# Kernel tuning notes

Measured on AMD Instinct MI355X. Metric: run time of the kernel, lower is better.

The kernel has to match this reference:

```python
import jax, jax.numpy as jnp
import numpy as np

B, C = 2048, 512          # batch, channels
CHG = 16                  # coarse grid side (16x16 -> N=256)
FHG = 16                  # fine grid side (16x16 -> F=256)
N = CHG * CHG             # coarse_span.total
F = FHG * FHG             # fine_total
K = 4                     # top4 sample mode
LOG_F = float(np.log(F))


def _ln(x, g, b, eps=1e-5):
    m = jnp.mean(x, axis=-1, keepdims=True)
    v = jnp.var(x, axis=-1, keepdims=True)
    return (x - m) * jax.lax.rsqrt(v + eps) * g + b


def _mlp3(x, w1, b1, w2, b2, w3, b3):
    # linear_stack: Linear+gelu, Linear+gelu, Linear (dropout=0 / eval)
    h = jax.nn.gelu(x @ w1 + b1)
    h = jax.nn.gelu(h @ w2 + b2)
    return h @ w3 + b3


def setup_inputs() -> dict:
    key = jax.random.key(0)
    ks = jax.random.split(key, 10)
    s = 0.02
    return {
        'x': jax.random.normal(ks[0], (B, C), jnp.float32),
        'in_g': jnp.ones((C,), jnp.float32), 'in_b': jnp.zeros((C,), jnp.float32),
        'nop_w': jax.random.normal(ks[1], (C, 1), jnp.float32) * s,
        'nop_b': jnp.zeros((1,), jnp.float32),
        'c_w1': jax.random.normal(ks[2], (C, C), jnp.float32) * s,
        'c_b1': jnp.zeros((C,), jnp.float32),
        'c_w2': jax.random.normal(ks[3], (C, C), jnp.float32) * s,
        'c_b2': jnp.zeros((C,), jnp.float32),
        'c_w3': jax.random.normal(ks[4], (C, N), jnp.float32) * s,
        'c_b3': jnp.zeros((N,), jnp.float32),
        'emb': jax.random.normal(ks[5], (N, C), jnp.float32),
        'emb_g': jnp.ones((C,), jnp.float32), 'emb_b': jnp.zeros((C,), jnp.float32),
        'f_w1': jax.random.normal(ks[6], (2 * C, C), jnp.float32) * s,
        'f_b1': jnp.zeros((C,), jnp.float32),
        'f_w2': jax.random.normal(ks[7], (C, C), jnp.float32) * s,
        'f_b2': jnp.zeros((C,), jnp.float32),
        'f_w3': jax.random.normal(ks[8], (C, F), jnp.float32) * s,
        'f_b3': jnp.zeros((F,), jnp.float32),
    }


def reference(x, in_g, in_b, nop_w, nop_b, c_w1, c_b1, c_w2, c_b2, c_w3, c_b3,
              emb, emb_g, emb_b, f_w1, f_b1, f_w2, f_b2, f_w3, f_b3):
    xn = _ln(x, in_g, in_b)                                  # (B,C)
    no_op = xn @ nop_w + nop_b                               # (B,1)
    coarse = _mlp3(xn, c_w1, c_b1, c_w2, c_b2, c_w3, c_b3)   # (B,N)
    _, idx = jax.lax.top_k(coarse, K)                        # (B,K) int32
    e = _ln(emb[idx], emb_g, emb_b)                          # (B,K,C)
    fin = jnp.concatenate([jnp.broadcast_to(xn[:, None, :], (B, K, C)), e], axis=-1)
    fine = _mlp3(fin, f_w1, f_b1, f_w2, f_b2, f_w3, f_b3)    # (B,K,F)
    # scatter value: coarse[b,i] - log F + fine + log F - lse(fine) = coarse[b,i] + log_softmax(fine)
    vals = jnp.take_along_axis(coarse, idx, axis=1)[:, :, None] + jax.nn.log_softmax(fine, axis=-1)
    dense = jnp.broadcast_to((coarse - LOG_F)[:, :, None], (B, N, F))
    dense = dense.at[jnp.arange(B)[:, None], idx].set(vals)  # top-k indices are distinct
    # view (B, ch0, ch1, fh0, fh1) -> permute (0,1,3,2,4) -> flatten
    xname = dense.reshape(B, CHG, CHG, FHG, FHG).transpose(0, 1, 3, 2, 4).reshape(B, -1)
    return jnp.concatenate([no_op, xname], axis=-1)          # (B, 1 + N*F)
```

## Files before the change

### kernel.cpp

```cpp
#include <hip/hip_runtime.h>
#include <math.h>

#define BATCH 2048
#define CH 512
#define N_COARSE 256
#define F_FINE 256
#define K_TOP 4
#define OUT_STRIDE 65537

typedef unsigned short ushort_t;
typedef __bf16 bf16x8 __attribute__((ext_vector_type(8)));
typedef float f32x4 __attribute__((ext_vector_type(4)));

typedef __attribute__((address_space(3))) unsigned int lds_uint;
typedef __attribute__((address_space(1))) unsigned int gl_uint;

__device__ __forceinline__ void gload_lds16(const ushort_t* g, ushort_t* l) {
    __builtin_amdgcn_global_load_lds((const gl_uint*)g, (lds_uint*)l, 16, 0, 0);
}

__device__ __forceinline__ float gelu_tanh(float x) {
    float x3 = x * x * x;
    float t = tanhf(0.7978845608028654f * (x + 0.044715f * x3));
    return 0.5f * x * (1.0f + t);
}

__device__ __forceinline__ ushort_t f2bf(float f) {
    unsigned u = __float_as_uint(f);
    unsigned r = (u + 0x7FFF + ((u >> 16) & 1)) >> 16;
    return (ushort_t)r;
}
__device__ __forceinline__ float bf2f(ushort_t h) {
    return __uint_as_float(((unsigned)h) << 16);
}

struct Params {
    const float *x, *in_g, *in_b, *nop_w, *nop_b;
    const float *c_w1, *c_b1, *c_w2, *c_b2, *c_w3, *c_b3;
    const float *emb, *emb_g, *emb_b;
    const float *f_w1, *f_b1, *f_w2, *f_b2, *f_w3, *f_b3;
    float *coarse, *out, *cvals;
    ushort_t *xnsp, *h1sp, *h2sp, *e_bf, *fh1_bf, *fh2_bf;
    ushort_t *wt1, *wt2, *wt3, *cwt1, *cwt2, *cwt3;
    int *idxb;
};

__global__ __launch_bounds__(256) void prep_kernel(Params p) {
    __shared__ float s[32][33];
    int u = blockIdx.x, t = threadIdx.x;
    if (u < 1536) {
        const float* W; ushort_t* Wt; int Kd, Nd, gx, gy; bool split;
        if (u < 512)       { W=p.f_w1; Wt=p.wt1; Kd=1024; Nd=512; gx=u&15; gy=u>>4; split=false; }
        else if (u < 768)  { int v=u-512;  W=p.f_w2; Wt=p.wt2; Kd=512; Nd=512; gx=v&15; gy=v>>4; split=false; }
        else if (u < 896)  { int v=u-768;  W=p.f_w3; Wt=p.wt3; Kd=512; Nd=256; gx=v&7;  gy=v>>3; split=false; }
        else if (u < 1152) { int v=u-896;  W=p.c_w1; Wt=p.cwt1; Kd=512; Nd=512; gx=v&15; gy=v>>4; split=true; }
        else if (u < 1408) { int v=u-1152; W=p.c_w2; Wt=p.cwt2; Kd=512; Nd=512; gx=v&15; gy=v>>4; split=true; }
        else               { int v=u-1408; W=p.c_w3; Wt=p.cwt3; Kd=512; Nd=256; gx=v&7;  gy=v>>3; split=true; }
        int tx = t & 31, ty = t >> 5;
        int n0 = gx * 32, k0 = gy * 32;
        #pragma unroll
        for (int i = 0; i < 4; ++i) {
            int r = ty + i * 8;
            s[r][tx] = W[(size_t)(k0 + r) * Nd + n0 + tx];
        }
        __syncthreads();
        if (!split) {
            #pragma unroll
            for (int i = 0; i < 4; ++i) {
                int r = ty + i * 8;
                Wt[(size_t)(n0 + r) * Kd + k0 + tx] = f2bf(s[tx][r]);
            }
        } else {
            #pragma unroll
            for (int i = 0; i < 4; ++i) {
                int r = ty + i * 8;
                float v = s[tx][r];
                ushort_t h = f2bf(v);
                Wt[(size_t)(n0 + r) * 1024 + k0 + tx] = h;
                Wt[(size_t)(n0 + r) * 1024 + 512 + k0 + tx] = f2bf(v - bf2f(h));
            }
        }
    } else {
        float* red = &s[0][0];
        int row = u - 1536;
        int lane = t & 63, wave = t >> 6;
        const float* xr = p.x + (size_t)row * CH;
        float v0 = xr[t], v1 = xr[t + 256];
        float sm = v0 + v1, ss = v0 * v0 + v1 * v1;
        #pragma unroll
        for (int off = 32; off; off >>= 1) { sm += __shfl_xor(sm, off); ss += __shfl_xor(ss, off); }
        if (lane == 0) { red[wave] = sm; red[4 + wave] = ss; }
        __syncthreads();
        sm = red[0] + red[1] + red[2] + red[3];
        ss = red[4] + red[5] + red[6] + red[7];
        float mean = sm * (1.0f / CH);
        float var = ss * (1.0f / CH) - mean * mean;
        float rsq = rsqrtf(var + 1e-5f);
        float xn0 = (v0 - mean) * rsq * p.in_g[t] + p.in_b[t];
        float xn1 = (v1 - mean) * rsq * p.in_g[t + 256] + p.in_b[t + 256];
        ushort_t* xr2 = p.xnsp + (size_t)row * 1024;
        ushort_t h0 = f2bf(xn0), h1v = f2bf(xn1);
        xr2[t] = h0; xr2[t + 256] = h1v;
        xr2[512 + t] = f2bf(xn0 - bf2f(h0));
        xr2[512 + t + 256] = f2bf(xn1 - bf2f(h1v));
        float d = xn0 * p.nop_w[t] + xn1 * p.nop_w[t + 256];
        #pragma unroll
        for (int off = 32; off; off >>= 1) d += __shfl_xor(d, off);
        __syncthreads();
        if (lane == 0) red[wave] = d;
        __syncthreads();
        if (t == 0) p.out[(size_t)row * OUT_STRIDE] = red[0] + red[1] + red[2] + red[3] + p.nop_b[0];
    }
}

template<bool SKIP>
__device__ __forceinline__ void bg_scatter_unit(const float* __restrict__ coarse,
                                                const int* __restrict__ idxb,
                                                float* __restrict__ out, int gu) {
    const float LOG_F = 5.545177444479562f;
    int b = gu >> 4, cx = gu & 15, t = threadIdx.x;
    int4 ii = SKIP ? *(const int4*)&idxb[b * 4] : make_int4(-1, -1, -1, -1);
    size_t rowb = (size_t)b * OUT_STRIDE + 1;
    const float* cr = coarse + (size_t)b * N_COARSE;
    #pragma unroll
    for (int q = 0; q < 4; ++q) {
        int o = cx * 4096 + q * 1024 + t * 4;
        int n = ((o >> 12) << 4) | ((o >> 4) & 15);
        bool skip = SKIP && ((n == ii.x) | (n == ii.y) | (n == ii.z) | (n == ii.w));
        if (!skip) {
            float base = cr[n] - LOG_F;
            float* op = out + rowb + o;
            __builtin_nontemporal_store(base, op + 0);
            __builtin_nontemporal_store(base, op + 1);
            __builtin_nontemporal_store(base, op + 2);
            __builtin_nontemporal_store(base, op + 3);
        }
    }
}

template<int MODE, int MT, int NT, int OUTM>
__global__ __launch_bounds__(256) void mfma_gemm_kernel(
    const ushort_t* __restrict__ A1, const ushort_t* __restrict__ A2,
    const ushort_t* __restrict__ Wt, const float* __restrict__ bias,
    const float* __restrict__ cvals, void* __restrict__ Cout, int Nd, int Ktot,
    const float* __restrict__ coarseB, const int* __restrict__ idxbB,
    float* __restrict__ outB, int gemmY, int suBase)
{
    if ((int)blockIdx.y >= gemmY) {
        int gu = suBase + ((int)blockIdx.y - gemmY) * (int)gridDim.x + (int)blockIdx.x;
        bg_scatter_unit<true>(coarseB, idxbB, outB, gu);
        return;
    }
    constexpr int FI = MT / 32, FJ = NT / 32;
    __shared__ ushort_t As[2][MT * 32];
    __shared__ ushort_t Bs[2][NT * 32];
    __shared__ float mxs[64 * 2];
    __shared__ float ses[64 * 2];
    int t = threadIdx.x;
    int n0 = blockIdx.x * NT, m0 = blockIdx.y * MT;
    int wave = t >> 6, lane = t & 63;
    int wm = (wave & 1) * (MT / 2), wn = (wave >> 1) * (NT / 2);
    int lr = lane & 15, quad = lane >> 4;
    int wbase = wave * 64;

    f32x4 acc[FI][FJ] = {};

    auto stageAB = [&](int k0, int pp) {
        int aoff = (MODE == 2) ? ((k0 >= 1024) ? k0 - 512 : (k0 & 511)) : k0;
        int woff = (MODE == 2) ? ((k0 >= 1024) ? k0 - 1024 : k0) : k0;
        constexpr int AL = MT * 4;
        constexpr int BL = NT * 4;
        if constexpr (AL >= 256) {
            #pragma unroll
            for (int i = 0; i < AL / 256; ++i) {
                int c = i * 256 + t, r = c >> 2, q = (c & 3) * 8;
                int gr = m0 + r;
                const ushort_t* ap;
                if (MODE == 1)      ap = (k0 < 512) ? A1 + (size_t)(gr >> 2) * 1024 + k0 + q
                                                    : A2 + (size_t)gr * 512 + (k0 - 512) + q;
                else if (MODE == 2) ap = A1 + (size_t)gr * 1024 + aoff + q;
                else                ap = A1 + (size_t)gr * Ktot + k0 + q;
                gload_lds16(ap, &As[pp][(i * 256 + wbase) * 8]);
            }
        } else {
            if (t < AL) {
                int c = t, r = c >> 2, q = (c & 3) * 8;
                int gr = m0 + r;
                const ushort_t* ap;
                if (MODE == 1)      ap = (k0 < 512) ? A1 + (size_t)(gr >> 2) * 1024 + k0 + q
                                                    : A2 + (size_t)gr * 512 + (k0 - 512) + q;
                else if (MODE == 2) ap = A1 + (size_t)gr * 1024 + aoff + q;
                else                ap = A1 + (size_t)gr * Ktot + k0 + q;
                gload_lds16(ap, &As[pp][wbase * 8]);
            }
        }
        if constexpr (BL >= 256) {
            #pragma unroll
            for (int i = 0; i < BL / 256; ++i) {
                int c = i * 256 + t, r = c >> 2, q = (c & 3) * 8;
                size_t wstride = (MODE == 2) ? 1024 : (size_t)Ktot;
                const ushort_t* bp = Wt + (size_t)(n0 + r) * wstride + woff + q;
                gload_lds16(bp, &Bs[pp][(i * 256 + wbase) * 8]);
            }
        } else {
            if (t < BL) {
                int c = t, r = c >> 2, q = (c & 3) * 8;
                size_t wstride = (MODE == 2) ? 1024 : (size_t)Ktot;
                const ushort_t* bp = Wt + (size_t)(n0 + r) * wstride + woff + q;
                gload_lds16(bp, &Bs[pp][wbase * 8]);
            }
        }
    };

    stageAB(0, 0);
    int steps = Ktot >> 5;
    int p = 0;
    for (int s = 0; s < steps; ++s) {
        __syncthreads();
        if (s + 1 < steps) stageAB((s + 1) * 32, p ^ 1);
        bf16x8 af[FI], bfr[FJ];
        #pragma unroll
        for (int i = 0; i < FI; ++i)
            af[i] = *(const bf16x8*)&As[p][(wm + i * 16 + lr) * 32 + quad * 8];
        #pragma unroll
        for (int j = 0; j < FJ; ++j)
            bfr[j] = *(const bf16x8*)&Bs[p][(wn + j * 16 + lr) * 32 + quad * 8];
        #pragma unroll
        for (int i = 0; i < FI; ++i)
            #pragma unroll
            for (int j = 0; j < FJ; ++j)
                acc[i][j] = __builtin_amdgcn_mfma_f32_16x16x32_bf16(af[i], bfr[j], acc[i][j], 0, 0, 0);
        p ^= 1;
    }

    if (OUTM == 3) {
        float bv[FJ];
        #pragma unroll
        for (int j = 0; j < FJ; ++j) bv[j] = bias[wn + j * 16 + lr];
        int half = wave >> 1;
        float rmx[FI][4];
        #pragma unroll
        for (int i = 0; i < FI; ++i)
            #pragma unroll
            for (int r = 0; r < 4; ++r) {
                float m = -1e30f;
                #pragma unroll
                for (int j = 0; j < FJ; ++j) m = fmaxf(m, acc[i][j][r] + bv[j]);
                #pragma unroll
                for (int mk = 1; mk < 16; mk <<= 1) m = fmaxf(m, __shfl_xor(m, mk));
                if (lr == 0) mxs[(wm + i * 16 + quad * 4 + r) * 2 + half] = m;
            }
        __syncthreads();
        #pragma unroll
        for (int i = 0; i < FI; ++i)
            #pragma unroll
            for (int r = 0; r < 4; ++r) {
                int rl = wm + i * 16 + quad * 4 + r;
                rmx[i][r] = fmaxf(mxs[rl * 2], mxs[rl * 2 + 1]);
            }
        #pragma unroll
        for (int i = 0; i < FI; ++i)
            #pragma unroll
            for (int r = 0; r < 4; ++r) {
                float sv = 0.f;
                #pragma unroll
                for (int j = 0; j < FJ; ++j) sv += expf(acc[i][j][r] + bv[j] - rmx[i][r]);
                #pragma unroll
                for (int mk = 1; mk < 16; mk <<= 1) sv += __shfl_xor(sv, mk);
                if (lr == 0) ses[(wm + i * 16 + quad * 4 + r) * 2 + half] = sv;
            }
        __syncthreads();
        #pragma unroll
        for (int i = 0; i < FI; ++i)
            #pragma unroll
            for (int r = 0; r < 4; ++r) {
                int rl = wm + i * 16 + quad * 4 + r;
                float se = ses[rl * 2] + ses[rl * 2 + 1];
                float addc = cvals[m0 + rl] - rmx[i][r] - logf(se);
                int m = m0 + rl;
                int n = idxbB[m];
                size_t base = (size_t)(m >> 2) * OUT_STRIDE + 1
                            + (size_t)((n >> 4) * 4096 + (n & 15) * 16);
                #pragma unroll
                for (int j = 0; j < FJ; ++j)
                    __builtin_nontemporal_store(acc[i][j][r] + bv[j] + addc,
                        &outB[base + (size_t)((wn >> 4) + j) * 256 + lr]);
            }
    } else {
        #pragma unroll
        for (int j = 0; j < FJ; ++j) {
            int col = n0 + wn + j * 16 + lr;
            float bvv = bias[col];
            #pragma unroll
            for (int i = 0; i < FI; ++i) {
                #pragma unroll
                for (int r = 0; r < 4; ++r) {
                    int row = m0 + wm + i * 16 + quad * 4 + r;
                    float val = acc[i][j][r] + bvv;
                    if (OUTM == 0) {
                        ((ushort_t*)Cout)[(size_t)row * Nd + col] = f2bf(gelu_tanh(val));
                    } else if (OUTM == 1) {
                        float gv = gelu_tanh(val);
                        ushort_t h = f2bf(gv);
                        ((ushort_t*)Cout)[(size_t)row * 1024 + col] = h;
                        ((ushort_t*)Cout)[(size_t)row * 1024 + 512 + col] = f2bf(gv - bf2f(h));
                    } else {
                        ((float*)Cout)[(size_t)row * Nd + col] = val;
                    }
                }
            }
        }
    }
}

__global__ __launch_bounds__(256) void topk_embln_kernel(Params p, int realX) {
    if ((int)blockIdx.x >= realX) {
        bg_scatter_unit<false>(p.coarse, nullptr, p.out, (int)blockIdx.x - realX);
        return;
    }
    __shared__ int sidx[4];
    int brow = blockIdx.x, t = threadIdx.x;
    int wave = t >> 6, lane = t & 63;
    if (wave == 0) {
        const float* cr = p.coarse + (size_t)brow * N_COARSE;
        float v[4]; int id[4];
        #pragma unroll
        for (int j = 0; j < 4; ++j) { v[j] = cr[lane + 64 * j]; id[j] = lane + 64 * j; }
        #pragma unroll
        for (int r = 0; r < K_TOP; ++r) {
            float bv = v[0]; int bi = id[0];
            #pragma unroll
            for (int j = 1; j < 4; ++j)
                if (v[j] > bv || (v[j] == bv && id[j] < bi)) { bv = v[j]; bi = id[j]; }
            #pragma unroll
            for (int off = 32; off; off >>= 1) {
                float ov = __shfl_xor(bv, off); int oi = __shfl_xor(bi, off);
                if (ov > bv || (ov == bv && oi < bi)) { bv = ov; bi = oi; }
            }
            if ((bi & 63) == lane) v[bi >> 6] = -INFINITY;
            if (lane == 0) {
                sidx[r] = bi;
                p.idxb[brow * K_TOP + r] = bi;
                p.cvals[brow * K_TOP + r] = bv;
            }
        }
    }
    __syncthreads();
    int n = sidx[wave];
    const float* er = p.emb + (size_t)n * CH + lane * 8;
    float4 u0 = *(const float4*)er;
    float4 u1 = *(const float4*)(er + 4);
    float s  = u0.x + u0.y + u0.z + u0.w + u1.x + u1.y + u1.z + u1.w;
    float ss = u0.x * u0.x + u0.y * u0.y + u0.z * u0.z + u0.w * u0.w
             + u1.x * u1.x + u1.y * u1.y + u1.z * u1.z + u1.w * u1.w;
    #pragma unroll
    for (int off = 32; off; off >>= 1) { s += __shfl_xor(s, off); ss += __shfl_xor(ss, off); }
    float mean = s * (1.0f / CH);
    float var = ss * (1.0f / CH) - mean * mean;
    float rsq = rsqrtf(var + 1e-5f);
    float4 g0 = *(const float4*)(p.emb_g + lane * 8), g1 = *(const float4*)(p.emb_g + lane * 8 + 4);
    float4 b0 = *(const float4*)(p.emb_b + lane * 8), b1 = *(const float4*)(p.emb_b + lane * 8 + 4);
    uint4 pk;
    pk.x = (unsigned)f2bf((u0.x - mean) * rsq * g0.x + b0.x) |
           ((unsigned)f2bf((u0.y - mean) * rsq * g0.y + b0.y) << 16);
    pk.y = (unsigned)f2bf((u0.z - mean) * rsq * g0.z + b0.z) |
           ((unsigned)f2bf((u0.w - mean) * rsq * g0.w + b0.w) << 16);
    pk.z = (unsigned)f2bf((u1.x - mean) * rsq * g1.x + b1.x) |
           ((unsigned)f2bf((u1.y - mean) * rsq * g1.y + b1.y) << 16);
    pk.w = (unsigned)f2bf((u1.z - mean) * rsq * g1.z + b1.z) |
           ((unsigned)f2bf((u1.w - mean) * rsq * g1.w + b1.w) << 16);
    *(uint4*)(p.e_bf + (size_t)(brow * K_TOP + wave) * CH + lane * 8) = pk;
}

extern "C" void kernel_launch(void* const* d_in, const int* in_sizes, int n_in,
                              void* d_out, int out_size, void* d_ws, size_t ws_size,
                              hipStream_t stream) {
    Params prm;
    prm.x     = (const float*)d_in[0];
    prm.in_g  = (const float*)d_in[1];
    prm.in_b  = (const float*)d_in[2];
    prm.nop_w = (const float*)d_in[3];
    prm.nop_b = (const float*)d_in[4];
    prm.c_w1  = (const float*)d_in[5];
    prm.c_b1  = (const float*)d_in[6];
    prm.c_w2  = (const float*)d_in[7];
    prm.c_b2  = (const float*)d_in[8];
    prm.c_w3  = (const float*)d_in[9];
    prm.c_b3  = (const float*)d_in[10];
    prm.emb   = (const float*)d_in[11];
    prm.emb_g = (const float*)d_in[12];
    prm.emb_b = (const float*)d_in[13];
    prm.f_w1  = (const float*)d_in[14];
    prm.f_b1  = (const float*)d_in[15];
    prm.f_w2  = (const float*)d_in[16];
    prm.f_b2  = (const float*)d_in[17];
    prm.f_w3  = (const float*)d_in[18];
    prm.f_b3  = (const float*)d_in[19];

    float* ws = (float*)d_ws;
    prm.coarse  = ws;
    prm.xnsp    = (ushort_t*)(prm.coarse + 524288);
    prm.h1sp    = prm.xnsp + 2097152;
    prm.h2sp    = prm.h1sp + 2097152;
    prm.e_bf    = prm.h2sp + 2097152;
    prm.fh1_bf  = prm.e_bf + 4194304;
    prm.fh2_bf  = prm.fh1_bf + 4194304;
    prm.wt1     = prm.fh2_bf + 4194304;
    prm.wt2     = prm.wt1 + 524288;
    prm.wt3     = prm.wt2 + 262144;
    prm.cwt1    = prm.wt3 + 131072;
    prm.cwt2    = prm.cwt1 + 524288;
    prm.cwt3    = prm.cwt2 + 524288;
    prm.idxb    = (int*)(prm.cwt3 + 262144);
    prm.cvals   = (float*)(prm.idxb + 8192);
    prm.out     = (float*)d_out;

    const int NOSC = 1 << 28;

    prep_kernel<<<3584, 256, 0, stream>>>(prm);
    mfma_gemm_kernel<2, 32, 64, 1><<<dim3(8, 64), 256, 0, stream>>>(
        prm.xnsp, nullptr, prm.cwt1, prm.c_b1, nullptr, prm.h1sp, 512, 1536,
        nullptr, nullptr, nullptr, NOSC, 0);
    mfma_gemm_kernel<2, 32, 64, 1><<<dim3(8, 64), 256, 0, stream>>>(
        prm.h1sp, nullptr, prm.cwt2, prm.c_b2, nullptr, prm.h2sp, 512, 1536,
        nullptr, nullptr, nullptr, NOSC, 0);
    mfma_gemm_kernel<2, 32, 32, 2><<<dim3(8, 64), 256, 0, stream>>>(
        prm.h2sp, nullptr, prm.cwt3, prm.c_b3, nullptr, prm.coarse, 256, 1536,
        nullptr, nullptr, nullptr, NOSC, 0);
    topk_embln_kernel<<<BATCH + 4096, 256, 0, stream>>>(prm, BATCH);
    mfma_gemm_kernel<1, 64, 64, 0><<<dim3(8, 128 + 1536), 256, 0, stream>>>(
        prm.xnsp, prm.e_bf, prm.wt1, prm.f_b1, nullptr, prm.fh1_bf, 512, 1024,
        prm.coarse, prm.idxb, prm.out, 128, 4096);
    mfma_gemm_kernel<0, 64, 64, 0><<<dim3(8, 128 + 1280), 256, 0, stream>>>(
        prm.fh1_bf, nullptr, prm.wt2, prm.f_b2, nullptr, prm.fh2_bf, 512, 512,
        prm.coarse, prm.idxb, prm.out, 128, 16384);
    mfma_gemm_kernel<0, 32, 256, 3><<<dim3(1, 256 + 6144), 256, 0, stream>>>(
        prm.fh2_bf, nullptr, prm.wt3, prm.f_b3, prm.cvals, nullptr, 256, 512,
        prm.coarse, prm.idxb, prm.out, 256, 26624);
}
```

Before: 680.9 us.

## Fuse prep, coarse MLP GEMMs and top-k into one persistent kernel with grid barriers

Replaces the five front-stage launches (prep, three coarse GEMMs, top-k/embedding LN plus background scatter) with a single persistent kernel of 512 blocks. Stages are separated by atomic-counter grid barriers, with a memset to reset the counter. The aim is to remove per-launch overhead and tail gaps between small kernels. The cost is spin-wait barriers, reduced parallelism in the prep and scatter phases, and a deadlock risk if the 512 blocks are not all co-resident (launch bounds of 256 threads, 2 blocks per SM).

```diff
diff --git a/kernel.cpp b/kernel.cpp
--- a/kernel.cpp
+++ b/kernel.cpp
@@ -45,9 +45,21 @@
     int *idxb;
 };
 
-__global__ __launch_bounds__(256) void prep_kernel(Params p) {
-    __shared__ float s[32][33];
-    int u = blockIdx.x, t = threadIdx.x;
+__device__ __forceinline__ void gbar(int* cnt, int target) {
+    __syncthreads();
+    if (threadIdx.x == 0) {
+        __threadfence();
+        atomicAdd(cnt, 1);
+        while (__hip_atomic_load(cnt, __ATOMIC_RELAXED, __HIP_MEMORY_SCOPE_AGENT) < target)
+            __builtin_amdgcn_s_sleep(8);
+        __threadfence();
+    }
+    __syncthreads();
+}
+
+__device__ __forceinline__ void prep_unit(const Params& p, int u, void* smemraw) {
+    float (*s)[33] = (float(*)[33])smemraw;
+    int t = threadIdx.x;
     if (u < 1536) {
         const float* W; ushort_t* Wt; int Kd, Nd, gx, gy; bool split;
         if (u < 512)       { W=p.f_w1; Wt=p.wt1; Kd=1024; Nd=512; gx=u&15; gy=u>>4; split=false; }
@@ -111,215 +123,84 @@
         __syncthreads();
         if (t == 0) p.out[(size_t)row * OUT_STRIDE] = red[0] + red[1] + red[2] + red[3] + p.nop_b[0];
     }
-}
-
-template<bool SKIP>
-__device__ __forceinline__ void bg_scatter_unit(const float* __restrict__ coarse,
-                                                const int* __restrict__ idxb,
-                                                float* __restrict__ out, int gu) {
-    const float LOG_F = 5.545177444479562f;
-    int b = gu >> 4, cx = gu & 15, t = threadIdx.x;
-    int4 ii = SKIP ? *(const int4*)&idxb[b * 4] : make_int4(-1, -1, -1, -1);
-    size_t rowb = (size_t)b * OUT_STRIDE + 1;
-    const float* cr = coarse + (size_t)b * N_COARSE;
-    #pragma unroll
-    for (int q = 0; q < 4; ++q) {
-        int o = cx * 4096 + q * 1024 + t * 4;
-        int n = ((o >> 12) << 4) | ((o >> 4) & 15);
-        bool skip = SKIP && ((n == ii.x) | (n == ii.y) | (n == ii.z) | (n == ii.w));
-        if (!skip) {
-            float base = cr[n] - LOG_F;
-            float* op = out + rowb + o;
-            __builtin_nontemporal_store(base, op + 0);
-            __builtin_nontemporal_store(base, op + 1);
-            __builtin_nontemporal_store(base, op + 2);
-            __builtin_nontemporal_store(base, op + 3);
-        }
-    }
-}
-
-template<int MODE, int MT, int NT, int OUTM>
-__global__ __launch_bounds__(256) void mfma_gemm_kernel(
-    const ushort_t* __restrict__ A1, const ushort_t* __restrict__ A2,
-    const ushort_t* __restrict__ Wt, const float* __restrict__ bias,
-    const float* __restrict__ cvals, void* __restrict__ Cout, int Nd, int Ktot,
-    const float* __restrict__ coarseB, const int* __restrict__ idxbB,
-    float* __restrict__ outB, int gemmY, int suBase)
+    __syncthreads();
+}
+
+template<int NT, int OUTM>
+__device__ __forceinline__ void coarse_tile(const ushort_t* __restrict__ A1,
+        const ushort_t* __restrict__ Wt, const float* __restrict__ bias,
+        void* __restrict__ Cout, int Nd, int n0, int m0, void* smemraw)
 {
-    if ((int)blockIdx.y >= gemmY) {
-        int gu = suBase + ((int)blockIdx.y - gemmY) * (int)gridDim.x + (int)blockIdx.x;
-        bg_scatter_unit<true>(coarseB, idxbB, outB, gu);
-        return;
-    }
-    constexpr int FI = MT / 32, FJ = NT / 32;
-    __shared__ ushort_t As[2][MT * 32];
-    __shared__ ushort_t Bs[2][NT * 32];
-    __shared__ float mxs[64 * 2];
-    __shared__ float ses[64 * 2];
+    constexpr int MT = 32;
+    constexpr int FJ = NT / 32;
+    ushort_t (*As)[MT * 32] = (ushort_t(*)[MT * 32])smemraw;
+    ushort_t (*Bs)[NT * 32] = (ushort_t(*)[NT * 32])((char*)smemraw + 2 * MT * 32 * 2);
     int t = threadIdx.x;
-    int n0 = blockIdx.x * NT, m0 = blockIdx.y * MT;
     int wave = t >> 6, lane = t & 63;
-    int wm = (wave & 1) * (MT / 2), wn = (wave >> 1) * (NT / 2);
+    int wm = (wave & 1) * 16, wn = (wave >> 1) * (NT / 2);
     int lr = lane & 15, quad = lane >> 4;
     int wbase = wave * 64;
 
-    f32x4 acc[FI][FJ] = {};
+    f32x4 acc[FJ] = {};
 
     auto stageAB = [&](int k0, int pp) {
-        int aoff = (MODE == 2) ? ((k0 >= 1024) ? k0 - 512 : (k0 & 511)) : k0;
-        int woff = (MODE == 2) ? ((k0 >= 1024) ? k0 - 1024 : k0) : k0;
-        constexpr int AL = MT * 4;
+        int aoff = (k0 >= 1024) ? k0 - 512 : (k0 & 511);
+        int woff = (k0 >= 1024) ? k0 - 1024 : k0;
+        if (t < MT * 4) {
+            int r = t >> 2, q = (t & 3) * 8;
+            gload_lds16(A1 + (size_t)(m0 + r) * 1024 + aoff + q, &As[pp][wbase * 8]);
+        }
         constexpr int BL = NT * 4;
-        if constexpr (AL >= 256) {
-            #pragma unroll
-            for (int i = 0; i < AL / 256; ++i) {
-                int c = i * 256 + t, r = c >> 2, q = (c & 3) * 8;
-                int gr = m0 + r;
-                const ushort_t* ap;
-                if (MODE == 1)      ap = (k0 < 512) ? A1 + (size_t)(gr >> 2) * 1024 + k0 + q
-                                                    : A2 + (size_t)gr * 512 + (k0 - 512) + q;
-                else if (MODE == 2) ap = A1 + (size_t)gr * 1024 + aoff + q;
-                else                ap = A1 + (size_t)gr * Ktot + k0 + q;
-                gload_lds16(ap, &As[pp][(i * 256 + wbase) * 8]);
-            }
+        if constexpr (BL >= 256) {
+            gload_lds16(Wt + (size_t)(n0 + (t >> 2)) * 1024 + woff + (t & 3) * 8,
+                        &Bs[pp][wbase * 8]);
         } else {
-            if (t < AL) {
-                int c = t, r = c >> 2, q = (c & 3) * 8;
-                int gr = m0 + r;
-                const ushort_t* ap;
-                if (MODE == 1)      ap = (k0 < 512) ? A1 + (size_t)(gr >> 2) * 1024 + k0 + q
-                                                    : A2 + (size_t)gr * 512 + (k0 - 512) + q;
-                else if (MODE == 2) ap = A1 + (size_t)gr * 1024 + aoff + q;
-                else                ap = A1 + (size_t)gr * Ktot + k0 + q;
-                gload_lds16(ap, &As[pp][wbase * 8]);
-            }
-        }
-        if constexpr (BL >= 256) {
-            #pragma unroll
-            for (int i = 0; i < BL / 256; ++i) {
-                int c = i * 256 + t, r = c >> 2, q = (c & 3) * 8;
-                size_t wstride = (MODE == 2) ? 1024 : (size_t)Ktot;
-                const ushort_t* bp = Wt + (size_t)(n0 + r) * wstride + woff + q;
-                gload_lds16(bp, &Bs[pp][(i * 256 + wbase) * 8]);
-            }
-        } else {
-            if (t < BL) {
-                int c = t, r = c >> 2, q = (c & 3) * 8;
-                size_t wstride = (MODE == 2) ? 1024 : (size_t)Ktot;
-                const ushort_t* bp = Wt + (size_t)(n0 + r) * wstride + woff + q;
-                gload_lds16(bp, &Bs[pp][wbase * 8]);
-            }
+            if (t < BL)
+                gload_lds16(Wt + (size_t)(n0 + (t >> 2)) * 1024 + woff + (t & 3) * 8,
+                            &Bs[pp][wbase * 8]);
         }
     };
 
     stageAB(0, 0);
-    int steps = Ktot >> 5;
-    int p = 0;
-    for (int s = 0; s < steps; ++s) {
-        __syncthreads();
-        if (s + 1 < steps) stageAB((s + 1) * 32, p ^ 1);
-        bf16x8 af[FI], bfr[FJ];
-        #pragma unroll
-        for (int i = 0; i < FI; ++i)
-            af[i] = *(const bf16x8*)&As[p][(wm + i * 16 + lr) * 32 + quad * 8];
+    int pbuf = 0;
+    for (int s = 0; s < 48; ++s) {
+        __syncthreads();
+        if (s + 1 < 48) stageAB((s + 1) * 32, pbuf ^ 1);
+        bf16x8 af = *(const bf16x8*)&As[pbuf][(wm + lr) * 32 + quad * 8];
+        bf16x8 bfr[FJ];
         #pragma unroll
         for (int j = 0; j < FJ; ++j)
-            bfr[j] = *(const bf16x8*)&Bs[p][(wn + j * 16 + lr) * 32 + quad * 8];
-        #pragma unroll
-        for (int i = 0; i < FI; ++i)
-            #pragma unroll
-            for (int j = 0; j < FJ; ++j)
-                acc[i][j] = __builtin_amdgcn_mfma_f32_16x16x32_bf16(af[i], bfr[j], acc[i][j], 0, 0, 0);
-        p ^= 1;
-    }
-
-    if (OUTM == 3) {
-        float bv[FJ];
-        #pragma unroll
-        for (int j = 0; j < FJ; ++j) bv[j] = bias[wn + j * 16 + lr];
-        int half = wave >> 1;
-        float rmx[FI][4];
-        #pragma unroll
-        for (int i = 0; i < FI; ++i)
-            #pragma unroll
-            for (int r = 0; r < 4; ++r) {
-                float m = -1e30f;
-                #pragma unroll
-                for (int j = 0; j < FJ; ++j) m = fmaxf(m, acc[i][j][r] + bv[j]);
-                #pragma unroll
-                for (int mk = 1; mk < 16; mk <<= 1) m = fmaxf(m, __shfl_xor(m, mk));
-                if (lr == 0) mxs[(wm + i * 16 + quad * 4 + r) * 2 + half] = m;
-            }
-        __syncthreads();
-        #pragma unroll
-        for (int i = 0; i < FI; ++i)
-            #pragma unroll
-            for (int r = 0; r < 4; ++r) {
-                int rl = wm + i * 16 + quad * 4 + r;
-                rmx[i][r] = fmaxf(mxs[rl * 2], mxs[rl * 2 + 1]);
-            }
-        #pragma unroll
-        for (int i = 0; i < FI; ++i)
-            #pragma unroll
-            for (int r = 0; r < 4; ++r) {
-                float sv = 0.f;
-                #pragma unroll
-                for (int j = 0; j < FJ; ++j) sv += expf(acc[i][j][r] + bv[j] - rmx[i][r]);
-                #pragma unroll
-                for (int mk = 1; mk < 16; mk <<= 1) sv += __shfl_xor(sv, mk);
-                if (lr == 0) ses[(wm + i * 16 + quad * 4 + r) * 2 + half] = sv;
-            }
-        __syncthreads();
-        #pragma unroll
-        for (int i = 0; i < FI; ++i)
-            #pragma unroll
-            for (int r = 0; r < 4; ++r) {
-                int rl = wm + i * 16 + quad * 4 + r;
-                float se = ses[rl * 2] + ses[rl * 2 + 1];
-                float addc = cvals[m0 + rl] - rmx[i][r] - logf(se);
-                int m = m0 + rl;
-                int n = idxbB[m];
-                size_t base = (size_t)(m >> 2) * OUT_STRIDE + 1
-                            + (size_t)((n >> 4) * 4096 + (n & 15) * 16);
-                #pragma unroll
-                for (int j = 0; j < FJ; ++j)
-                    __builtin_nontemporal_store(acc[i][j][r] + bv[j] + addc,
-                        &outB[base + (size_t)((wn >> 4) + j) * 256 + lr]);
-            }
-    } else {
-        #pragma unroll
-        for (int j = 0; j < FJ; ++j) {
-            int col = n0 + wn + j * 16 + lr;
-            float bvv = bias[col];
-            #pragma unroll
-            for (int i = 0; i < FI; ++i) {
-                #pragma unroll
-                for (int r = 0; r < 4; ++r) {
-                    int row = m0 + wm + i * 16 + quad * 4 + r;
-                    float val = acc[i][j][r] + bvv;
-                    if (OUTM == 0) {
-                        ((ushort_t*)Cout)[(size_t)row * Nd + col] = f2bf(gelu_tanh(val));
-                    } else if (OUTM == 1) {
-                        float gv = gelu_tanh(val);
-                        ushort_t h = f2bf(gv);
-                        ((ushort_t*)Cout)[(size_t)row * 1024 + col] = h;
-                        ((ushort_t*)Cout)[(size_t)row * 1024 + 512 + col] = f2bf(gv - bf2f(h));
-                    } else {
-                        ((float*)Cout)[(size_t)row * Nd + col] = val;
-                    }
-                }
-            }
-        }
-    }
-}
-
-__global__ __launch_bounds__(256) void topk_embln_kernel(Params p, int realX) {
-    if ((int)blockIdx.x >= realX) {
-        bg_scatter_unit<false>(p.coarse, nullptr, p.out, (int)blockIdx.x - realX);
-        return;
-    }
-    __shared__ int sidx[4];
-    int brow = blockIdx.x, t = threadIdx.x;
+            bfr[j] = *(const bf16x8*)&Bs[pbuf][(wn + j * 16 + lr) * 32 + quad * 8];
+        #pragma unroll
+        for (int j = 0; j < FJ; ++j)
+            acc[j] = __builtin_amdgcn_mfma_f32_16x16x32_bf16(af, bfr[j], acc[j], 0, 0, 0);
+        pbuf ^= 1;
+    }
+
+    #pragma unroll
+    for (int j = 0; j < FJ; ++j) {
+        int col = n0 + wn + j * 16 + lr;
+        float bvv = bias[col];
+        #pragma unroll
+        for (int r = 0; r < 4; ++r) {
+            int row = m0 + wm + quad * 4 + r;
+            float val = acc[j][r] + bvv;
+            if (OUTM == 1) {
+                float gv = gelu_tanh(val);
+                ushort_t h = f2bf(gv);
+                ((ushort_t*)Cout)[(size_t)row * 1024 + col] = h;
+                ((ushort_t*)Cout)[(size_t)row * 1024 + 512 + col] = f2bf(gv - bf2f(h));
+            } else {
+                ((float*)Cout)[(size_t)row * Nd + col] = val;
+            }
+        }
+    }
+    __syncthreads();
+}
+
+__device__ __forceinline__ void topk_unit(const Params& p, int brow, void* smemraw) {
+    int* sidx = (int*)smemraw;
+    int t = threadIdx.x;
     int wave = t >> 6, lane = t & 63;
     if (wave == 0) {
         const float* cr = p.coarse + (size_t)brow * N_COARSE;
@@ -370,6 +251,209 @@
     pk.w = (unsigned)f2bf((u1.z - mean) * rsq * g1.z + b1.z) |
            ((unsigned)f2bf((u1.w - mean) * rsq * g1.w + b1.w) << 16);
     *(uint4*)(p.e_bf + (size_t)(brow * K_TOP + wave) * CH + lane * 8) = pk;
+    __syncthreads();
+}
+
+template<bool SKIP>
+__device__ __forceinline__ void bg_scatter_unit(const float* __restrict__ coarse,
+                                                const int* __restrict__ idxb,
+                                                float* __restrict__ out, int gu) {
+    const float LOG_F = 5.545177444479562f;
+    int b = gu >> 4, cx = gu & 15, t = threadIdx.x;
+    int4 ii = SKIP ? *(const int4*)&idxb[b * 4] : make_int4(-1, -1, -1, -1);
+    size_t rowb = (size_t)b * OUT_STRIDE + 1;
+    const float* cr = coarse + (size_t)b * N_COARSE;
+    #pragma unroll
+    for (int q = 0; q < 4; ++q) {
+        int o = cx * 4096 + q * 1024 + t * 4;
+        int n = ((o >> 12) << 4) | ((o >> 4) & 15);
+        bool skip = SKIP && ((n == ii.x) | (n == ii.y) | (n == ii.z) | (n == ii.w));
+        if (!skip) {
+            float base = cr[n] - LOG_F;
+            float* op = out + rowb + o;
+            __builtin_nontemporal_store(base, op + 0);
+            __builtin_nontemporal_store(base, op + 1);
+            __builtin_nontemporal_store(base, op + 2);
+            __builtin_nontemporal_store(base, op + 3);
+        }
+    }
+}
+
+__global__ __launch_bounds__(256, 2) void fused_front_kernel(Params p, int* barcnt) {
+    __shared__ __align__(16) unsigned char smem[12544];
+    int nb = (int)gridDim.x;
+    for (int u = blockIdx.x; u < 3584; u += nb) prep_unit(p, u, smem);
+    gbar(barcnt, nb);
+    for (int u = blockIdx.x; u < 512; u += nb)
+        coarse_tile<64, 1>(p.xnsp, p.cwt1, p.c_b1, p.h1sp, 512, (u & 7) * 64, (u >> 3) * 32, smem);
+    gbar(barcnt, 2 * nb);
+    for (int u = blockIdx.x; u < 512; u += nb)
+        coarse_tile<64, 1>(p.h1sp, p.cwt2, p.c_b2, p.h2sp, 512, (u & 7) * 64, (u >> 3) * 32, smem);
+    gbar(barcnt, 3 * nb);
+    for (int u = blockIdx.x; u < 512; u += nb)
+        coarse_tile<32, 2>(p.h2sp, p.cwt3, p.c_b3, p.coarse, 256, (u & 7) * 32, (u >> 3) * 32, smem);
+    gbar(barcnt, 4 * nb);
+    for (int r = blockIdx.x; r < BATCH; r += nb) topk_unit(p, r, smem);
+    for (int gu = blockIdx.x; gu < 4096; gu += nb)
+        bg_scatter_unit<false>(p.coarse, nullptr, p.out, gu);
+}
+
+template<int MODE, int MT, int NT, int OUTM>
+__global__ __launch_bounds__(256) void mfma_gemm_kernel(
+    const ushort_t* __restrict__ A1, const ushort_t* __restrict__ A2,
+    const ushort_t* __restrict__ Wt, const float* __restrict__ bias,
+    const float* __restrict__ cvals, void* __restrict__ Cout, int Nd, int Ktot,
+    const float* __restrict__ coarseB, const int* __restrict__ idxbB,
+    float* __restrict__ outB, int gemmY, int suBase)
+{
+    if ((int)blockIdx.y >= gemmY) {
+        int gu = suBase + ((int)blockIdx.y - gemmY) * (int)gridDim.x + (int)blockIdx.x;
+        bg_scatter_unit<true>(coarseB, idxbB, outB, gu);
+        return;
+    }
+    constexpr int FI = MT / 32, FJ = NT / 32;
+    __shared__ ushort_t As[2][MT * 32];
+    __shared__ ushort_t Bs[2][NT * 32];
+    __shared__ float mxs[64 * 2];
+    __shared__ float ses[64 * 2];
+    int t = threadIdx.x;
+    int n0 = blockIdx.x * NT, m0 = blockIdx.y * MT;
+    int wave = t >> 6, lane = t & 63;
+    int wm = (wave & 1) * (MT / 2), wn = (wave >> 1) * (NT / 2);
+    int lr = lane & 15, quad = lane >> 4;
+    int wbase = wave * 64;
+
+    f32x4 acc[FI][FJ] = {};
+
+    auto stageAB = [&](int k0, int pp) {
+        constexpr int AL = MT * 4;
+        constexpr int BL = NT * 4;
+        if constexpr (AL >= 256) {
+            #pragma unroll
+            for (int i = 0; i < AL / 256; ++i) {
+                int c = i * 256 + t, r = c >> 2, q = (c & 3) * 8;
+                int gr = m0 + r;
+                const ushort_t* ap;
+                if (MODE == 1)      ap = (k0 < 512) ? A1 + (size_t)(gr >> 2) * 1024 + k0 + q
+                                                    : A2 + (size_t)gr * 512 + (k0 - 512) + q;
+                else                ap = A1 + (size_t)gr * Ktot + k0 + q;
+                gload_lds16(ap, &As[pp][(i * 256 + wbase) * 8]);
+            }
+        } else {
+            if (t < AL) {
+                int r = t >> 2, q = (t & 3) * 8;
+                int gr = m0 + r;
+                const ushort_t* ap;
+                if (MODE == 1)      ap = (k0 < 512) ? A1 + (size_t)(gr >> 2) * 1024 + k0 + q
+                                                    : A2 + (size_t)gr * 512 + (k0 - 512) + q;
+                else                ap = A1 + (size_t)gr * Ktot + k0 + q;
+                gload_lds16(ap, &As[pp][wbase * 8]);
+            }
+        }
+        if constexpr (BL >= 256) {
+            #pragma unroll
+            for (int i = 0; i < BL / 256; ++i) {
+                int c = i * 256 + t, r = c >> 2, q = (c & 3) * 8;
+                gload_lds16(Wt + (size_t)(n0 + r) * Ktot + k0 + q, &Bs[pp][(i * 256 + wbase) * 8]);
+            }
+        } else {
+            if (t < BL) {
+                int r = t >> 2, q = (t & 3) * 8;
+                gload_lds16(Wt + (size_t)(n0 + r) * Ktot + k0 + q, &Bs[pp][wbase * 8]);
+            }
+        }
+    };
+
+    stageAB(0, 0);
+    int steps = Ktot >> 5;
+    int p = 0;
+    for (int s = 0; s < steps; ++s) {
+        __syncthreads();
+        if (s + 1 < steps) stageAB((s + 1) * 32, p ^ 1);
+        bf16x8 af[FI], bfr[FJ];
+        #pragma unroll
+        for (int i = 0; i < FI; ++i)
+            af[i] = *(const bf16x8*)&As[p][(wm + i * 16 + lr) * 32 + quad * 8];
+        #pragma unroll
+        for (int j = 0; j < FJ; ++j)
+            bfr[j] = *(const bf16x8*)&Bs[p][(wn + j * 16 + lr) * 32 + quad * 8];
+        #pragma unroll
+        for (int i = 0; i < FI; ++i)
+            #pragma unroll
+            for (int j = 0; j < FJ; ++j)
+                acc[i][j] = __builtin_amdgcn_mfma_f32_16x16x32_bf16(af[i], bfr[j], acc[i][j], 0, 0, 0);
+        p ^= 1;
+    }
+
+    if (OUTM == 3) {
+        float bv[FJ];
+        #pragma unroll
+        for (int j = 0; j < FJ; ++j) bv[j] = bias[wn + j * 16 + lr];
+        int half = wave >> 1;
+        float rmx[FI][4];
+        #pragma unroll
+        for (int i = 0; i < FI; ++i)
+            #pragma unroll
+            for (int r = 0; r < 4; ++r) {
+                float m = -1e30f;
+                #pragma unroll
+                for (int j = 0; j < FJ; ++j) m = fmaxf(m, acc[i][j][r] + bv[j]);
+                #pragma unroll
+                for (int mk = 1; mk < 16; mk <<= 1) m = fmaxf(m, __shfl_xor(m, mk));
+                if (lr == 0) mxs[(wm + i * 16 + quad * 4 + r) * 2 + half] = m;
+            }
+        __syncthreads();
+        #pragma unroll
+        for (int i = 0; i < FI; ++i)
+            #pragma unroll
+            for (int r = 0; r < 4; ++r) {
+                int rl = wm + i * 16 + quad * 4 + r;
+                rmx[i][r] = fmaxf(mxs[rl * 2], mxs[rl * 2 + 1]);
+            }
+        #pragma unroll
+        for (int i = 0; i < FI; ++i)
+            #pragma unroll
+            for (int r = 0; r < 4; ++r) {
+                float sv = 0.f;
+                #pragma unroll
+                for (int j = 0; j < FJ; ++j) sv += expf(acc[i][j][r] + bv[j] - rmx[i][r]);
+                #pragma unroll
+                for (int mk = 1; mk < 16; mk <<= 1) sv += __shfl_xor(sv, mk);
+                if (lr == 0) ses[(wm + i * 16 + quad * 4 + r) * 2 + half] = sv;
+            }
+        __syncthreads();
+        #pragma unroll
+        for (int i = 0; i < FI; ++i)
+            #pragma unroll
+            for (int r = 0; r < 4; ++r) {
+                int rl = wm + i * 16 + quad * 4 + r;
+                float se = ses[rl * 2] + ses[rl * 2 + 1];
+                float addc = cvals[m0 + rl] - rmx[i][r] - logf(se);
+                int m = m0 + rl;
+                int n = idxbB[m];
+                size_t base = (size_t)(m >> 2) * OUT_STRIDE + 1
+                            + (size_t)((n >> 4) * 4096 + (n & 15) * 16);
+                #pragma unroll
+                for (int j = 0; j < FJ; ++j)
+                    __builtin_nontemporal_store(acc[i][j][r] + bv[j] + addc,
+                        &outB[base + (size_t)((wn >> 4) + j) * 256 + lr]);
+            }
+    } else {
+        #pragma unroll
+        for (int j = 0; j < FJ; ++j) {
+            int col = n0 + wn + j * 16 + lr;
+            float bvv = bias[col];
+            #pragma unroll
+            for (int i = 0; i < FI; ++i) {
+                #pragma unroll
+                for (int r = 0; r < 4; ++r) {
+                    int row = m0 + wm + i * 16 + quad * 4 + r;
+                    float val = acc[i][j][r] + bvv;
+                    ((ushort_t*)Cout)[(size_t)row * Nd + col] = f2bf(gelu_tanh(val));
+                }
+            }
+        }
+    }
 }
 
 extern "C" void kernel_launch(void* const* d_in, const int* in_sizes, int n_in,
@@ -414,20 +498,10 @@
     prm.idxb    = (int*)(prm.cwt3 + 262144);
     prm.cvals   = (float*)(prm.idxb + 8192);
     prm.out     = (float*)d_out;
-
-    const int NOSC = 1 << 28;
-
-    prep_kernel<<<3584, 256, 0, stream>>>(prm);
-    mfma_gemm_kernel<2, 32, 64, 1><<<dim3(8, 64), 256, 0, stream>>>(
-        prm.xnsp, nullptr, prm.cwt1, prm.c_b1, nullptr, prm.h1sp, 512, 1536,
-        nullptr, nullptr, nullptr, NOSC, 0);
-    mfma_gemm_kernel<2, 32, 64, 1><<<dim3(8, 64), 256, 0, stream>>>(
-        prm.h1sp, nullptr, prm.cwt2, prm.c_b2, nullptr, prm.h2sp, 512, 1536,
-        nullptr, nullptr, nullptr, NOSC, 0);
-    mfma_gemm_kernel<2, 32, 32, 2><<<dim3(8, 64), 256, 0, stream>>>(
-        prm.h2sp, nullptr, prm.cwt3, prm.c_b3, nullptr, prm.coarse, 256, 1536,
-        nullptr, nullptr, nullptr, NOSC, 0);
-    topk_embln_kernel<<<BATCH + 4096, 256, 0, stream>>>(prm, BATCH);
+    int* barcnt = (int*)(prm.cvals + 8192);
+
+    hipMemsetAsync(barcnt, 0, 16, stream);
+    fused_front_kernel<<<512, 256, 0, stream>>>(prm, barcnt);
     mfma_gemm_kernel<1, 64, 64, 0><<<dim3(8, 128 + 1536), 256, 0, stream>>>(
         prm.xnsp, prm.e_bf, prm.wt1, prm.f_b1, nullptr, prm.fh1_bf, 512, 1024,
         prm.coarse, prm.idxb, prm.out, 128, 4096);
```

Measured after the change: 874.5 us. +28.4%, slower.
